# Performance work log

Hardware: AMD Instinct MI355X
Metric: run time of the kernel (lower is better)

Reference implementation:

```python
import jax, jax.numpy as jnp
import numpy as np

N = 100000
E = 1600000
NEG_SLOPE = 0.2
DEPTH = 5


def setup_inputs() -> dict:
    key = jax.random.key(0)
    ks = jax.random.split(key, 8)
    x = jax.random.normal(ks[0], (N, 100), dtype=jnp.float32)
    edge_index = jax.random.randint(ks[1], (2, E), 0, N, dtype=jnp.int64)
    # layer 0: 100 -> 48; layers 1..4: 48 -> 48
    W0 = jax.random.normal(ks[2], (100, 48), dtype=jnp.float32) * 0.1
    Wrest = jax.random.normal(ks[3], (DEPTH - 1, 48, 48), dtype=jnp.float32) * 0.1
    a_src = jax.random.normal(ks[4], (DEPTH, 48), dtype=jnp.float32) * 0.1
    a_dst = jax.random.normal(ks[5], (DEPTH, 48), dtype=jnp.float32) * 0.1
    bias = jax.random.normal(ks[6], (DEPTH, 48), dtype=jnp.float32) * 0.1
    return {"x": x, "edge_index": edge_index, "W0": W0, "Wrest": Wrest,
            "a_src": a_src, "a_dst": a_dst, "bias": bias}


def _gat_layer(x, src, dst, W, a_s, a_d, b):
    h = x @ W                                   # [N, F]
    alpha_s = h @ a_s                           # [N]
    alpha_d = h @ a_d                           # [N]
    e = alpha_s[src] + alpha_d[dst]             # [E']
    e = jax.nn.leaky_relu(e, NEG_SLOPE)
    # segment softmax over edges grouped by destination node
    m = jax.ops.segment_max(e, dst, num_segments=N)
    m = jnp.where(jnp.isfinite(m), m, 0.0)      # empty segments -> 0
    p = jnp.exp(e - m[dst])
    s = jax.ops.segment_sum(p, dst, num_segments=N)
    alpha = p / jnp.maximum(s[dst], 1e-16)      # [E']
    out = jax.ops.segment_sum(alpha[:, None] * h[src], dst, num_segments=N)
    return out + b


def reference(x, edge_index, W0, Wrest, a_src, a_dst, bias):
    # PyG GATConv default add_self_loops=True
    loops = jnp.arange(N, dtype=edge_index.dtype)
    src = jnp.concatenate([edge_index[0], loops])
    dst = jnp.concatenate([edge_index[1], loops])
    Ws = [W0] + [Wrest[i] for i in range(DEPTH - 1)]
    h = x
    for l in range(DEPTH):
        h = _gat_layer(h, src, dst, Ws[l], a_src[l], a_dst[l], bias[l])
        h = jax.nn.elu(h)
    return h
```

## Files before the change

kernel.cpp:

```cpp
#include <hip/hip_runtime.h>

#define NN 100000
#define EE 1600000
#define ETOT (EE + NN)
#define FF 48
#define NEG 0.2f
#define BSH 9
#define BNODES 512
#define NBUK ((NN + BNODES - 1) / BNODES)
#define TILE 2048


__global__ __launch_bounds__(256) void k_bhist(const int* __restrict__ ei,
                                               int* __restrict__ bcnt) {
    __shared__ int h[256];
    int t = threadIdx.x;
    h[t] = 0;
    __syncthreads();
    for (int i = blockIdx.x * 256 + t; i < ETOT; i += gridDim.x * 256) {
        int dd = (i < EE) ? ei[EE + i] : (i - EE);
        atomicAdd(&h[dd >> BSH], 1);
    }
    __syncthreads();
    if (h[t] > 0) atomicAdd(&bcnt[t], h[t]);
}

__global__ void k_bscan(const int* __restrict__ bcnt, int* __restrict__ boff,
                        int* __restrict__ bcur) {
    __shared__ int sb[256];
    int t = threadIdx.x;
    int v = (t < NBUK) ? bcnt[t] : 0;
    sb[t] = v;
    __syncthreads();
    for (int o = 1; o < 256; o <<= 1) {
        int x = (t >= o) ? sb[t - o] : 0;
        __syncthreads();
        sb[t] += x;
        __syncthreads();
    }
    int excl = sb[t] - v;
    boff[t] = excl;
    bcur[t] = excl;
}

__global__ __launch_bounds__(256) void k_bscatter(const int* __restrict__ ei,
                                                  int* __restrict__ bcur,
                                                  int2* __restrict__ pairs) {
    __shared__ int hist[256], incl[256], exc[256], curv[256], gb[256];
    __shared__ int2 stage[TILE];
    __shared__ int staddr[TILE];
    int t = threadIdx.x;
    hist[t] = 0;
    __syncthreads();
    int base = blockIdx.x * TILE;
    int s[8], d[8], b[8];
#pragma unroll
    for (int j = 0; j < 8; j++) {
        int i = base + t + j * 256;
        if (i < ETOT) {
            int ss, dd;
            if (i < EE) { ss = ei[i]; dd = ei[EE + i]; }
            else { ss = i - EE; dd = ss; }
            s[j] = ss; d[j] = dd; b[j] = dd >> BSH;
            atomicAdd(&hist[b[j]], 1);
        } else {
            b[j] = -1;
        }
    }
    __syncthreads();
    int hv = hist[t];
    incl[t] = hv;
    __syncthreads();
    for (int o = 1; o < 256; o <<= 1) {
        int x = (t >= o) ? incl[t - o] : 0;
        __syncthreads();
        incl[t] += x;
        __syncthreads();
    }
    int excl = incl[t] - hv;
    exc[t] = excl;
    curv[t] = excl;
    if (hv > 0) gb[t] = atomicAdd(&bcur[t], hv);
    __syncthreads();
    int total = incl[255];
#pragma unroll
    for (int j = 0; j < 8; j++) {
        if (b[j] >= 0) {
            int pos = atomicAdd(&curv[b[j]], 1);
            stage[pos] = make_int2(s[j], d[j]);
            staddr[pos] = gb[b[j]] + (pos - exc[b[j]]);
        }
    }
    __syncthreads();
    for (int i = t; i < total; i += 256) pairs[staddr[i]] = stage[i];
}

__global__ __launch_bounds__(256) void k_bfill(const int2* __restrict__ pairs,
                                               const int* __restrict__ boff,
                                               int* __restrict__ off,
                                               int* __restrict__ ssrc) {
    __shared__ int cnt[BNODES], cu[BNODES], sb[256];
    int blk = blockIdx.x;
    int t = threadIdx.x;
    int n0 = blk << BSH;
    int beg = boff[blk], end = boff[blk + 1];
    cnt[t] = 0;
    cnt[t + 256] = 0;
    __syncthreads();
    for (int i = beg + t; i < end; i += 256) {
        atomicAdd(&cnt[pairs[i].y - n0], 1);
    }
    __syncthreads();
    int c0 = cnt[2 * t], c1 = cnt[2 * t + 1];
    sb[t] = c0 + c1;
    __syncthreads();
    for (int o = 1; o < 256; o <<= 1) {
        int x = (t >= o) ? sb[t - o] : 0;
        __syncthreads();
        sb[t] += x;
        __syncthreads();
    }
    int e2 = sb[t] - (c0 + c1);
    cu[2 * t] = e2;
    cu[2 * t + 1] = e2 + c0;
    int n1 = min(n0 + BNODES, NN);
    if (n0 + 2 * t < n1) off[n0 + 2 * t] = beg + e2;
    if (n0 + 2 * t + 1 < n1) off[n0 + 2 * t + 1] = beg + e2 + c0;
    if (blk == 0 && t == 0) off[NN] = ETOT;
    __syncthreads();
    for (int i = beg + t; i < end; i += 256) {
        int2 pr = pairs[i];
        int pos = atomicAdd(&cu[pr.y - n0], 1);
        ssrc[beg + pos] = pr.x;
    }
}


template <int K, int KC, int R>
__global__ __launch_bounds__(256) void k_gemm(const float* __restrict__ in,
                                              const float* __restrict__ W,
                                              const float* __restrict__ a_s,
                                              const float* __restrict__ a_d,
                                              float* __restrict__ h,
                                              float* __restrict__ as_,
                                              float* __restrict__ ad_) {
    __shared__ float Wl[K * FF];
    __shared__ float asl[FF], adl[FF];
    int t = threadIdx.x;
    for (int i = t; i < K * FF / 4; i += 256)
        ((float4*)Wl)[i] = ((const float4*)W)[i];
    if (t < FF) { asl[t] = a_s[t]; adl[t] = a_d[t]; }
    __syncthreads();

    int fg = t & 3;
    int pr = t >> 2;
    int r0 = blockIdx.x * (64 * R) + pr * R;
    if (r0 >= NN) return;

    constexpr int NC = K / KC;
    constexpr int QC = KC / 4;
    const float4* x4 = (const float4*)in;
    const float4* wl4 = (const float4*)Wl;

    float acc[R][12];
#pragma unroll
    for (int r = 0; r < R; r++)
#pragma unroll
        for (int j = 0; j < 12; j++) acc[r][j] = 0.f;

    for (int c = 0; c < NC; c++) {
        float xs[R][KC];
#pragma unroll
        for (int r = 0; r < R; r++) {
#pragma unroll
            for (int q = 0; q < QC; q++) {
                float4 v = x4[(size_t)(r0 + r) * (K / 4) + c * QC + q];
                xs[r][4 * q + 0] = v.x; xs[r][4 * q + 1] = v.y;
                xs[r][4 * q + 2] = v.z; xs[r][4 * q + 3] = v.w;
            }
        }
#pragma unroll
        for (int kk = 0; kk < KC; kk++) {
            const int k = c * KC + kk;
            const float4 w0 = wl4[k * 12 + fg * 3 + 0];
            const float4 w1 = wl4[k * 12 + fg * 3 + 1];
            const float4 w2 = wl4[k * 12 + fg * 3 + 2];
#pragma unroll
            for (int r = 0; r < R; r++) {
                const float xv = xs[r][kk];
                acc[r][0] = fmaf(xv, w0.x, acc[r][0]);
                acc[r][1] = fmaf(xv, w0.y, acc[r][1]);
                acc[r][2] = fmaf(xv, w0.z, acc[r][2]);
                acc[r][3] = fmaf(xv, w0.w, acc[r][3]);
                acc[r][4] = fmaf(xv, w1.x, acc[r][4]);
                acc[r][5] = fmaf(xv, w1.y, acc[r][5]);
                acc[r][6] = fmaf(xv, w1.z, acc[r][6]);
                acc[r][7] = fmaf(xv, w1.w, acc[r][7]);
                acc[r][8] = fmaf(xv, w2.x, acc[r][8]);
                acc[r][9] = fmaf(xv, w2.y, acc[r][9]);
                acc[r][10] = fmaf(xv, w2.z, acc[r][10]);
                acc[r][11] = fmaf(xv, w2.w, acc[r][11]);
            }
        }
    }

#pragma unroll
    for (int r = 0; r < R; r++) {
        float4* hp = (float4*)(h + (size_t)(r0 + r) * FF + fg * 12);
        hp[0] = make_float4(acc[r][0], acc[r][1], acc[r][2], acc[r][3]);
        hp[1] = make_float4(acc[r][4], acc[r][5], acc[r][6], acc[r][7]);
        hp[2] = make_float4(acc[r][8], acc[r][9], acc[r][10], acc[r][11]);
    }

    float ps[R], pd[R];
#pragma unroll
    for (int r = 0; r < R; r++) { ps[r] = 0.f; pd[r] = 0.f; }
#pragma unroll
    for (int j = 0; j < 12; j++) {
        float av = asl[fg * 12 + j], dv = adl[fg * 12 + j];
#pragma unroll
        for (int r = 0; r < R; r++) {
            ps[r] = fmaf(acc[r][j], av, ps[r]);
            pd[r] = fmaf(acc[r][j], dv, pd[r]);
        }
    }
#pragma unroll
    for (int r = 0; r < R; r++) {
        ps[r] += __shfl_xor(ps[r], 1); ps[r] += __shfl_xor(ps[r], 2);
        pd[r] += __shfl_xor(pd[r], 1); pd[r] += __shfl_xor(pd[r], 2);
    }
    if (fg == 0) {
#pragma unroll
        for (int r = 0; r < R; r++) {
            as_[r0 + r] = ps[r];
            ad_[r0 + r] = pd[r];
        }
    }
}

template <bool LAST>
__global__ __launch_bounds__(256) void k_aggr_fused(
    const float* __restrict__ h, const float* __restrict__ as_,
    const float* __restrict__ ad_, const int* __restrict__ off,
    const int* __restrict__ ssrc, const float* __restrict__ bias_l,
    const float* __restrict__ Wn, const float* __restrict__ asn,
    const float* __restrict__ adn, float* __restrict__ hn,
    float* __restrict__ as_o, float* __restrict__ ad_o,
    float* __restrict__ out) {
    int wave = threadIdx.x >> 6;
    int lane = threadIdx.x & 63;
    int d = blockIdx.x * 4 + wave;
    if (d >= NN) return;
    int beg = __builtin_amdgcn_readfirstlane(off[d]);
    int end = __builtin_amdgcn_readfirstlane(off[d + 1]);
    int deg = end - beg;
    float add = ad_[d];
    int fW = (lane < FF) ? lane : lane - FF;
    unsigned foff = (unsigned)(fW * 4);
    const char* hb = (const char*)h;

    float acc = 0.f, s = 0.f;

    if (deg <= 64) {
        int srcb = 0;
        float e = -1e30f;
        if (lane < deg) {
            int src = ssrc[beg + lane];
            srcb = src * (FF * 4);
            float t = as_[src] + add;
            e = (t > 0.f) ? t : NEG * t;
        }
        float m = e;
#pragma unroll
        for (int o = 32; o; o >>= 1) m = fmaxf(m, __shfl_xor(m, o));
        float p = (lane < deg) ? __expf(e - m) : 0.f;
        float sv = p;
#pragma unroll
        for (int o = 32; o; o >>= 1) sv += __shfl_xor(sv, o);
        s = sv;

        unsigned pbits = __float_as_uint(p);
        int degR = (deg + 7) & ~7;
        for (int i = 0; i < degR; i += 8) {
            float pj[8], hv[8];
#pragma unroll
            for (int j = 0; j < 8; j++) {
                pj[j] = __uint_as_float(
                    (unsigned)__builtin_amdgcn_readlane((int)pbits, i + j));
                int sbj = __builtin_amdgcn_readlane(srcb, i + j);
                hv[j] = *(const float*)(hb + (unsigned)sbj + foff);
            }
#pragma unroll
            for (int j = 0; j < 8; j++) acc = fmaf(pj[j], hv[j], acc);
        }
    } else {
        float m = -1e30f;
        for (int i = beg + lane; i < end; i += 64) {
            float t = as_[ssrc[i]] + add;
            t = (t > 0.f) ? t : NEG * t;
            m = fmaxf(m, t);
        }
#pragma unroll
        for (int o = 32; o; o >>= 1) m = fmaxf(m, __shfl_xor(m, o));
        for (int i = beg; i < end; i++) {
            int src = ssrc[i];
            float e = as_[src] + add;
            e = (e > 0.f) ? e : NEG * e;
            float pp = __expf(e - m);
            s += pp;
            if (lane < FF) acc = fmaf(pp, h[(size_t)src * FF + lane], acc);
        }
    }

    float v = acc / fmaxf(s, 1e-16f) + bias_l[fW];
    float act = (v > 0.f) ? v : (__expf(v) - 1.0f);

    if (LAST) {
        if (lane < FF) out[(size_t)d * FF + lane] = act;
        return;
    }

    int g0 = __float_as_int(act);
    asm volatile("v_and_b32 %0, 0, %0" : "+v"(g0));
    const float* W1 = (const float*)((const char*)Wn + g0);

    float hn_acc = 0.f;
    {
        float w[24];
#pragma unroll
        for (int k = 0; k < 24; k++) w[k] = W1[k * FF + fW];
#pragma unroll
        for (int k = 0; k < 24; k++) {
            float av = __uint_as_float(
                (unsigned)__builtin_amdgcn_readlane(__float_as_int(act), k));
            hn_acc = fmaf(av, w[k], hn_acc);
        }
    }
    int g1 = __float_as_int(hn_acc);
    asm volatile("v_and_b32 %0, 0, %0" : "+v"(g1));
    const float* W2 = (const float*)((const char*)Wn + g1);
    {
        float w[24];
#pragma unroll
        for (int k = 0; k < 24; k++) w[k] = W2[(24 + k) * FF + fW];
#pragma unroll
        for (int k = 0; k < 24; k++) {
            float av = __uint_as_float(
                (unsigned)__builtin_amdgcn_readlane(__float_as_int(act), 24 + k));
            hn_acc = fmaf(av, w[k], hn_acc);
        }
    }

    float hz = (lane < FF) ? hn_acc : 0.f;
    float ps = hz * asn[fW];
    float pd = hz * adn[fW];
#pragma unroll
    for (int o = 32; o; o >>= 1) {
        ps += __shfl_xor(ps, o);
        pd += __shfl_xor(pd, o);
    }

    if (lane < FF) hn[(size_t)d * FF + lane] = hn_acc;
    if (lane == 0) { as_o[d] = ps; ad_o[d] = pd; }
}


static inline size_t alup(size_t x) { return (x + 255) & ~(size_t)255; }

extern "C" void kernel_launch(void* const* d_in, const int* in_sizes, int n_in,
                              void* d_out, int out_size, void* d_ws, size_t ws_size,
                              hipStream_t stream) {
    const float* x = (const float*)d_in[0];
    const int* ei = (const int*)d_in[1];
    const float* W0 = (const float*)d_in[2];
    const float* Wr = (const float*)d_in[3];
    const float* As = (const float*)d_in[4];
    const float* Ad = (const float*)d_in[5];
    const float* B = (const float*)d_in[6];
    float* out = (float*)d_out;

    char* p = (char*)d_ws;
    int* off = (int*)p;      p += alup((NN + 1) * sizeof(int));
    int* bcnt = (int*)p;     p += alup(256 * sizeof(int));
    int* boff = (int*)p;     p += alup(257 * sizeof(int));
    int* bcur = (int*)p;     p += alup(256 * sizeof(int));
    int2* pairs = (int2*)p;  p += alup((size_t)ETOT * sizeof(int2));
    int* ssrc = (int*)p;     p += alup((size_t)ETOT * sizeof(int) + 256);
    float* hA = (float*)p;   p += alup((size_t)NN * FF * sizeof(float) + 256);
    float* hB = (float*)p;   p += alup((size_t)NN * FF * sizeof(float) + 256);
    float* asA = (float*)p;  p += alup(NN * sizeof(float));
    float* adA = (float*)p;  p += alup(NN * sizeof(float));
    float* asB = (float*)p;  p += alup(NN * sizeof(float));
    float* adB = (float*)p;  p += alup(NN * sizeof(float));

    hipMemsetAsync(bcnt, 0, 256 * sizeof(int), stream);
    k_bhist<<<512, 256, 0, stream>>>(ei, bcnt);
    k_bscan<<<1, 256, 0, stream>>>(bcnt, boff, bcur);
    k_bscatter<<<(ETOT + TILE - 1) / TILE, 256, 0, stream>>>(ei, bcur, pairs);
    k_bfill<<<NBUK, 256, 0, stream>>>(pairs, boff, off, ssrc);

    int g0 = (NN + 127) / 128;
    k_gemm<100, 20, 2><<<g0, 256, 0, stream>>>(x, W0, As, Ad, hA, asA, adA);

    int gA = (NN + 3) / 4;
    k_aggr_fused<false><<<gA, 256, 0, stream>>>(hA, asA, adA, off, ssrc, B + 0,
                                                Wr + 0 * 2304, As + 48, Ad + 48,
                                                hB, asB, adB, nullptr);
    k_aggr_fused<false><<<gA, 256, 0, stream>>>(hB, asB, adB, off, ssrc, B + 48,
                                                Wr + 1 * 2304, As + 96, Ad + 96,
                                                hA, asA, adA, nullptr);
    k_aggr_fused<false><<<gA, 256, 0, stream>>>(hA, asA, adA, off, ssrc, B + 96,
                                                Wr + 2 * 2304, As + 144, Ad + 144,
                                                hB, asB, adB, nullptr);
    k_aggr_fused<false><<<gA, 256, 0, stream>>>(hB, asB, adB, off, ssrc, B + 144,
                                                Wr + 3 * 2304, As + 192, Ad + 192,
                                                hA, asA, adA, nullptr);
    k_aggr_fused<true><<<gA, 256, 0, stream>>>(hA, asA, adA, off, ssrc, B + 192,
                                               nullptr, nullptr, nullptr,
                                               nullptr, nullptr, nullptr, out);
}
```

Baseline: 472.8 us.

## Process four nodes per wave and keep next-layer weights in registers

Each wave now handles four destination nodes instead of one. The 48-row column of the next-layer weight matrix, plus the attention vectors and bias, is loaded into registers once per wave and reused across those nodes. The 48-term dot product is split into four independent accumulator chains to expose ILP. The old asm trick that serialized the weight loads is gone. In exchange, register pressure rises with w[48], which may lower occupancy, and there are a quarter as many waves to hide gather latency. The loop over four nodes per wave has no bounds guard, which only works because NN is divisible by 16.

Result: slower. 487.2 us (+3.1%).

```diff
diff --git a/kernel.cpp b/kernel.cpp
--- a/kernel.cpp
+++ b/kernel.cpp
@@ -249,119 +249,117 @@
     float* __restrict__ out) {
     int wave = threadIdx.x >> 6;
     int lane = threadIdx.x & 63;
-    int d = blockIdx.x * 4 + wave;
-    if (d >= NN) return;
-    int beg = __builtin_amdgcn_readfirstlane(off[d]);
-    int end = __builtin_amdgcn_readfirstlane(off[d + 1]);
-    int deg = end - beg;
-    float add = ad_[d];
+    int gid = blockIdx.x * 4 + wave;
+    if (gid * 4 >= NN) return;
     int fW = (lane < FF) ? lane : lane - FF;
     unsigned foff = (unsigned)(fW * 4);
     const char* hb = (const char*)h;
-
-    float acc = 0.f, s = 0.f;
-
-    if (deg <= 64) {
-        int srcb = 0;
-        float e = -1e30f;
-        if (lane < deg) {
-            int src = ssrc[beg + lane];
-            srcb = src * (FF * 4);
-            float t = as_[src] + add;
-            e = (t > 0.f) ? t : NEG * t;
-        }
-        float m = e;
-#pragma unroll
-        for (int o = 32; o; o >>= 1) m = fmaxf(m, __shfl_xor(m, o));
-        float p = (lane < deg) ? __expf(e - m) : 0.f;
-        float sv = p;
-#pragma unroll
-        for (int o = 32; o; o >>= 1) sv += __shfl_xor(sv, o);
-        s = sv;
-
-        unsigned pbits = __float_as_uint(p);
-        int degR = (deg + 7) & ~7;
-        for (int i = 0; i < degR; i += 8) {
-            float pj[8], hv[8];
-#pragma unroll
-            for (int j = 0; j < 8; j++) {
-                pj[j] = __uint_as_float(
-                    (unsigned)__builtin_amdgcn_readlane((int)pbits, i + j));
-                int sbj = __builtin_amdgcn_readlane(srcb, i + j);
-                hv[j] = *(const float*)(hb + (unsigned)sbj + foff);
-            }
-#pragma unroll
-            for (int j = 0; j < 8; j++) acc = fmaf(pj[j], hv[j], acc);
-        }
-    } else {
-        float m = -1e30f;
-        for (int i = beg + lane; i < end; i += 64) {
-            float t = as_[ssrc[i]] + add;
-            t = (t > 0.f) ? t : NEG * t;
-            m = fmaxf(m, t);
-        }
-#pragma unroll
-        for (int o = 32; o; o >>= 1) m = fmaxf(m, __shfl_xor(m, o));
-        for (int i = beg; i < end; i++) {
-            int src = ssrc[i];
-            float e = as_[src] + add;
-            e = (e > 0.f) ? e : NEG * e;
-            float pp = __expf(e - m);
-            s += pp;
-            if (lane < FF) acc = fmaf(pp, h[(size_t)src * FF + lane], acc);
-        }
-    }
-
-    float v = acc / fmaxf(s, 1e-16f) + bias_l[fW];
-    float act = (v > 0.f) ? v : (__expf(v) - 1.0f);
-
-    if (LAST) {
-        if (lane < FF) out[(size_t)d * FF + lane] = act;
-        return;
-    }
-
-    int g0 = __float_as_int(act);
-    asm volatile("v_and_b32 %0, 0, %0" : "+v"(g0));
-    const float* W1 = (const float*)((const char*)Wn + g0);
-
-    float hn_acc = 0.f;
-    {
-        float w[24];
-#pragma unroll
-        for (int k = 0; k < 24; k++) w[k] = W1[k * FF + fW];
-#pragma unroll
-        for (int k = 0; k < 24; k++) {
-            float av = __uint_as_float(
-                (unsigned)__builtin_amdgcn_readlane(__float_as_int(act), k));
-            hn_acc = fmaf(av, w[k], hn_acc);
-        }
-    }
-    int g1 = __float_as_int(hn_acc);
-    asm volatile("v_and_b32 %0, 0, %0" : "+v"(g1));
-    const float* W2 = (const float*)((const char*)Wn + g1);
-    {
-        float w[24];
-#pragma unroll
-        for (int k = 0; k < 24; k++) w[k] = W2[(24 + k) * FF + fW];
-#pragma unroll
-        for (int k = 0; k < 24; k++) {
-            float av = __uint_as_float(
-                (unsigned)__builtin_amdgcn_readlane(__float_as_int(act), 24 + k));
-            hn_acc = fmaf(av, w[k], hn_acc);
-        }
-    }
-
-    float hz = (lane < FF) ? hn_acc : 0.f;
-    float ps = hz * asn[fW];
-    float pd = hz * adn[fW];
-#pragma unroll
-    for (int o = 32; o; o >>= 1) {
-        ps += __shfl_xor(ps, o);
-        pd += __shfl_xor(pd, o);
-    }
-
-    if (lane < FF) hn[(size_t)d * FF + lane] = hn_acc;
-    if (lane == 0) { as_o[d] = ps; ad_o[d] = pd; }
+    float bias_v = bias_l[fW];
+
+    float w[48];
+    float asn_v = 0.f, adn_v = 0.f;
+    if (!LAST) {
+        asn_v = asn[fW];
+        adn_v = adn[fW];
+#pragma unroll
+        for (int k = 0; k < 48; k++) w[k] = Wn[k * FF + fW];
+    }
+
+    for (int n = 0; n < 4; n++) {
+        int d = gid * 4 + n;
+        int beg = __builtin_amdgcn_readfirstlane(off[d]);
+        int end = __builtin_amdgcn_readfirstlane(off[d + 1]);
+        int deg = end - beg;
+        float add = ad_[d];
+
+        float acc = 0.f, s = 0.f;
+
+        if (deg <= 64) {
+            int srcb = 0;
+            float e = -1e30f;
+            if (lane < deg) {
+                int src = ssrc[beg + lane];
+                srcb = src * (FF * 4);
+                float t = as_[src] + add;
+                e = (t > 0.f) ? t : NEG * t;
+            }
+            float m = e;
+#pragma unroll
+            for (int o = 32; o; o >>= 1) m = fmaxf(m, __shfl_xor(m, o));
+            float p = (lane < deg) ? __expf(e - m) : 0.f;
+            float sv = p;
+#pragma unroll
+            for (int o = 32; o; o >>= 1) sv += __shfl_xor(sv, o);
+            s = sv;
+
+            unsigned pbits = __float_as_uint(p);
+            int degR = (deg + 7) & ~7;
+            for (int i = 0; i < degR; i += 8) {
+                float pj[8], hv[8];
+#pragma unroll
+                for (int j = 0; j < 8; j++) {
+                    pj[j] = __uint_as_float(
+                        (unsigned)__builtin_amdgcn_readlane((int)pbits, i + j));
+                    int sbj = __builtin_amdgcn_readlane(srcb, i + j);
+                    hv[j] = *(const float*)(hb + (unsigned)sbj + foff);
+                }
+#pragma unroll
+                for (int j = 0; j < 8; j++) acc = fmaf(pj[j], hv[j], acc);
+            }
+        } else {
+            float m = -1e30f;
+            for (int i = beg + lane; i < end; i += 64) {
+                float t = as_[ssrc[i]] + add;
+                t = (t > 0.f) ? t : NEG * t;
+                m = fmaxf(m, t);
+            }
+#pragma unroll
+            for (int o = 32; o; o >>= 1) m = fmaxf(m, __shfl_xor(m, o));
+            for (int i = beg; i < end; i++) {
+                int src = ssrc[i];
+                float e = as_[src] + add;
+                e = (e > 0.f) ? e : NEG * e;
+                float pp = __expf(e - m);
+                s += pp;
+                if (lane < FF) acc = fmaf(pp, h[(size_t)src * FF + lane], acc);
+            }
+        }
+
+        float v = acc / fmaxf(s, 1e-16f) + bias_v;
+        float act = (v > 0.f) ? v : (__expf(v) - 1.0f);
+
+        if (LAST) {
+            if (lane < FF) out[(size_t)d * FF + lane] = act;
+            continue;
+        }
+
+        float c0 = 0.f, c1 = 0.f, c2 = 0.f, c3 = 0.f;
+        int ab = __float_as_int(act);
+#pragma unroll
+        for (int k = 0; k < 12; k++) {
+            float a0 = __uint_as_float((unsigned)__builtin_amdgcn_readlane(ab, k));
+            float a1 = __uint_as_float((unsigned)__builtin_amdgcn_readlane(ab, 12 + k));
+            float a2 = __uint_as_float((unsigned)__builtin_amdgcn_readlane(ab, 24 + k));
+            float a3 = __uint_as_float((unsigned)__builtin_amdgcn_readlane(ab, 36 + k));
+            c0 = fmaf(a0, w[k], c0);
+            c1 = fmaf(a1, w[12 + k], c1);
+            c2 = fmaf(a2, w[24 + k], c2);
+            c3 = fmaf(a3, w[36 + k], c3);
+        }
+        float hn_acc = (c0 + c1) + (c2 + c3);
+
+        float hz = (lane < FF) ? hn_acc : 0.f;
+        float ps = hz * asn_v;
+        float pd = hz * adn_v;
+#pragma unroll
+        for (int o = 32; o; o >>= 1) {
+            ps += __shfl_xor(ps, o);
+            pd += __shfl_xor(pd, o);
+        }
+
+        if (lane < FF) hn[(size_t)d * FF + lane] = hn_acc;
+        if (lane == 0) { as_o[d] = ps; ad_o[d] = pd; }
+    }
 }
 
 
@@ -402,7 +400,7 @@
     int g0 = (NN + 127) / 128;
     k_gemm<100, 20, 2><<<g0, 256, 0, stream>>>(x, W0, As, Ad, hA, asA, adA);
 
-    int gA = (NN + 3) / 4;
+    int gA = (NN + 15) / 16;
     k_aggr_fused<false><<<gA, 256, 0, stream>>>(hA, asA, adA, off, ssrc, B + 0,
                                                 Wr + 0 * 2304, As + 48, Ad + 48,
                                                 hB, asB, adB, nullptr);
```
